# Kernel tuning notes

Hardware: AMD Instinct MI355X
Metric: run time of the kernel (lower is better)

The kernel has to match this reference:

```python
import jax, jax.numpy as jnp
import numpy as np

N = 1024       # gaussians
H = 256
W = 256
C = 64         # spectral channels
K = 2          # gabor components per gaussian
RADIUS_CLIP = 1.0
CHOL_BOUND = np.array([0.5, 0.0, 0.5], dtype=np.float32)


def setup_inputs() -> dict:
    key = jax.random.key(0)
    k1, k2, k3, k4, k5 = jax.random.split(key, 5)
    # _xyz = atanh(2*(rand-0.5))
    u = jax.random.uniform(k1, (N, 2), minval=-0.999, maxval=0.999)
    xyz = jnp.arctanh(u)
    cholesky = jax.random.uniform(k2, (N, 3))
    opacity = jnp.ones((N, 1), dtype=jnp.float32)
    # features init: inverse_softplus(0.05) + 0.01*randn
    inv_sp = float(np.log(np.expm1(0.05)))
    features_dc = inv_sp + 0.01 * jax.random.normal(k3, (N, C))
    gabor_freqs = (jax.random.uniform(k4, (N * K, 2)) - 0.5) * 0.002
    gabor_weights = jax.random.uniform(k5, (N * K, 1)) * -5.0
    return {
        'xyz': xyz, 'cholesky': cholesky, 'opacity': opacity,
        'features_dc': features_dc, 'gabor_freqs': gabor_freqs,
        'gabor_weights': gabor_weights,
    }


def _render(xyz, cholesky, opacity, features_dc, gabor_freqs, gabor_weights):
    # --- project_gaussians_2d ---
    xy = jnp.tanh(xyz)                              # [N,2] in (-1,1)
    xs = 0.5 * W * (xy[:, 0] + 1.0)                 # pixel-space centers
    ys = 0.5 * H * (xy[:, 1] + 1.0)
    L = cholesky + jnp.asarray(CHOL_BOUND)[None, :]  # [N,3] -> l1,l2,l3
    l1, l2, l3 = L[:, 0], L[:, 1], L[:, 2]
    # Sigma = L L^T, L = [[l1,0],[l2,l3]]
    s11 = l1 * l1
    s12 = l1 * l2
    s22 = l2 * l2 + l3 * l3
    det = (l1 * l3) ** 2
    ca = s22 / det                                  # conic = Sigma^-1
    cb = -s12 / det
    cc = s11 / det
    # radius = ceil(3*sqrt(max eigenvalue)); prune tiny gaussians
    mid = 0.5 * (s11 + s22)
    lam_max = mid + jnp.sqrt(jnp.maximum(mid * mid - det, 1e-8))
    radius = jnp.ceil(3.0 * jnp.sqrt(lam_max))
    keep = (radius > RADIUS_CLIP).astype(xyz.dtype)  # [N]

    # --- rasterize_gabor_sum (dense reference; kernel tiles, math identical) ---
    px = jnp.arange(W, dtype=xyz.dtype) + 0.5
    py = jnp.arange(H, dtype=xyz.dtype) + 0.5
    pxf = jnp.tile(px, H)                            # [HW]
    pyf = jnp.repeat(py, W)                          # [HW]
    dx = xs[:, None] - pxf[None, :]                  # [N,HW]
    dy = ys[:, None] - pyf[None, :]
    sigma = 0.5 * (ca[:, None] * dx * dx + cc[:, None] * dy * dy) + cb[:, None] * dx * dy
    alpha = opacity * jnp.exp(-sigma) * keep[:, None]  # [N,HW]

    freqs = jnp.exp(gabor_freqs).reshape(N, K, 2)
    wts = jax.nn.sigmoid(gabor_weights).reshape(N, K)
    mod = jnp.ones_like(dx)
    for k in range(K):  # K=2, structurally small loop
        mod = mod + wts[:, k, None] * jnp.cos(freqs[:, k, 0, None] * dx + freqs[:, k, 1, None] * dy)

    wmap = alpha * mod                               # [N,HW]
    feats = jax.nn.softplus(features_dc)             # [N,C]
    out = jnp.einsum('np,nc->pc', wmap, feats)       # [HW,C], sum compositing
    out = jnp.clip(out, 0.0, 1.0)
    return out.reshape(1, H, W, C).transpose(0, 3, 1, 2)  # [1,C,H,W]


def reference(xyz, cholesky, opacity, features_dc, gabor_freqs, gabor_weights):
    return _render(xyz, cholesky, opacity, features_dc, gabor_freqs, gabor_weights)
```

## Files before the change

kernel.cpp:

```cpp
#include <hip/hip_runtime.h>
#include <hip/hip_bf16.h>

#define NG     1024
#define NC     64
#define CULL_T 15.0f
#define MAXL   256
#define APAD   258
#define L2E    1.44269504f
#define INV2PI 0.15915494f

typedef float    f32x4 __attribute__((ext_vector_type(4)));
typedef _Float16 f16x4 __attribute__((ext_vector_type(4)));
typedef _Float16 f16x2 __attribute__((ext_vector_type(2)));

__device__ __forceinline__ float wgt_f(float4 p0, float4 p1, float4 p2,
                                       float pxf, float pyf) {
    const float dx = p0.x - pxf, dy = p0.y - pyf;
    const float t  = fmaf(p0.w, dy, p0.z * dx);
    const float s2 = fmaf(p1.x * dy, dy, dx * t);
    const float e  = __builtin_amdgcn_exp2f(s2);
    const float r1 = fmaf(p2.x, dx, p2.y * dy);
    const float c1 = __builtin_amdgcn_cosf(__builtin_amdgcn_fractf(r1));
    const float r2 = fmaf(p2.z, dx, p2.w * dy);
    const float c2 = __builtin_amdgcn_cosf(__builtin_amdgcn_fractf(r2));
    const float m  = fmaf(p1.w, c2, fmaf(p1.z, c1, 1.f));
    return e * p1.y * m;
}

__global__ __launch_bounds__(512) void fused_mfma_kernel(
    const float* __restrict__ xyz,  const float* __restrict__ chol,
    const float* __restrict__ opac, const float* __restrict__ fdc,
    const float* __restrict__ gfrq, const float* __restrict__ gwts,
    float* __restrict__ out)
{
    __shared__ float4 s_p0[MAXL], s_p1[MAXL], s_p2[MAXL];
    __shared__ unsigned short s_list[MAXL];
    __shared__ int s_scnt[16];
    __shared__ _Float16 A_lds[NC][APAD];

    const int tid  = threadIdx.x;
    const int lane = tid & 63, w = tid >> 6;

    const int x0 = (blockIdx.x & 7) << 5;
    const int y0 = (blockIdx.x >> 3) << 3;
    const float xlo = x0 + 0.5f, xhi = x0 + 31.5f;
    const float ylo = y0 + 0.5f, yhi = y0 + 7.5f;

    float4 P0[2];
    float  NCC[2], OK[2];
    bool   lv[2];
    int    pos[2];
    #pragma unroll
    for (int r = 0; r < 2; ++r) {
        const int n = (r << 9) + tid;
        const float2 xy = ((const float2*)xyz)[n];
        const float ex = __builtin_amdgcn_exp2f(2.f * L2E * xy.x);
        const float ey = __builtin_amdgcn_exp2f(2.f * L2E * xy.y);
        const float xs = 256.f - 256.f * __builtin_amdgcn_rcpf(1.f + ex);
        const float ys = 256.f - 256.f * __builtin_amdgcn_rcpf(1.f + ey);

        const float l1 = chol[3*n]     + 0.5f;
        const float l2 = chol[3*n + 1];
        const float l3 = chol[3*n + 2] + 0.5f;
        const float s11 = l1*l1, s12 = l1*l2, s22 = l2*l2 + l3*l3;
        const float dt  = (l1*l3) * (l1*l3);
        const float inv = __builtin_amdgcn_rcpf(dt);
        const float na = -0.5f * L2E * s22 * inv;
        const float nb =          L2E * s12 * inv;
        const float nc = -0.5f * L2E * s11 * inv;
        const float mid = 0.5f * (s11 + s22);
        const float lam = mid + __builtin_amdgcn_sqrtf(fmaxf(mid*mid - dt, 1e-8f));
        const float radius = ceilf(3.f * __builtin_amdgcn_sqrtf(lam));
        const float keep = (radius > 1.0f) ? 1.f : 0.f;
        const float oK = opac[n] * keep;
        const float r2 = (oK != 0.f) ? (2.f * CULL_T * lam) : -1.f;

        const float nx = fminf(fmaxf(xs, xlo), xhi);
        const float ny = fminf(fmaxf(ys, ylo), yhi);
        const float ddx = xs - nx, ddy = ys - ny;
        lv[r] = (ddx*ddx + ddy*ddy) <= r2;

        const unsigned long long m = __ballot(lv[r]);
        pos[r] = __popcll(m & ((1ull << lane) - 1ull));
        if (lane == 0) s_scnt[(r << 3) + w] = __popcll(m);

        P0[r] = make_float4(xs, ys, na, nb);
        NCC[r] = nc; OK[r] = oK;
    }
    __syncthreads();

    int pre[17];
    pre[0] = 0;
    #pragma unroll
    for (int s = 0; s < 16; ++s) pre[s+1] = pre[s] + s_scnt[s];
    const int total = min(pre[16], MAXL);

    #pragma unroll
    for (int r = 0; r < 2; ++r) {
        if (lv[r]) {
            const int p = pre[(r << 3) + w] + pos[r];
            if (p < MAXL) {
                const int n = (r << 9) + tid;
                const float4 gf = ((const float4*)gfrq)[n];
                const float2 gw = ((const float2*)gwts)[n];
                s_list[p] = (unsigned short)n;
                s_p0[p] = P0[r];
                s_p1[p] = make_float4(NCC[r], OK[r],
                    __builtin_amdgcn_rcpf(1.f + __builtin_amdgcn_exp2f(-L2E*gw.x)),
                    __builtin_amdgcn_rcpf(1.f + __builtin_amdgcn_exp2f(-L2E*gw.y)));
                s_p2[p] = make_float4(
                    __builtin_amdgcn_exp2f(L2E*gf.x)*INV2PI,
                    __builtin_amdgcn_exp2f(L2E*gf.y)*INV2PI,
                    __builtin_amdgcn_exp2f(L2E*gf.z)*INV2PI,
                    __builtin_amdgcn_exp2f(L2E*gf.w)*INV2PI);
            }
        }
    }
    for (int idx = total + tid; idx < MAXL; idx += 512) {
        s_p0[idx] = make_float4(0,0,0,0);
        s_p1[idx] = make_float4(0,0,0,0);
        s_p2[idx] = make_float4(0,0,0,0);
    }
    __syncthreads();

    const int nkc = (total + 15) >> 4;

    {
        const int c = tid & 63, kq = tid >> 6;
        for (int i = 0; i < nkc; ++i) {
            const int k0 = (i << 4) + (kq << 1);
            float v0 = 0.f, v1 = 0.f;
            if (k0 < total) {
                const int n = (int)s_list[k0];
                const float x = fdc[(n << 6) + c];
                v0 = 0.69314718f * __builtin_amdgcn_logf(
                         1.f + __builtin_amdgcn_exp2f(L2E * x));
            }
            if (k0 + 1 < total) {
                const int n = (int)s_list[k0 + 1];
                const float x = fdc[(n << 6) + c];
                v1 = 0.69314718f * __builtin_amdgcn_logf(
                         1.f + __builtin_amdgcn_exp2f(L2E * x));
            }
            *(f16x2*)&A_lds[c][k0] = (f16x2){(_Float16)v0, (_Float16)v1};
        }
    }
    __syncthreads();

    const int c15 = lane & 15, g = lane >> 4;
    const float pxf0 = x0 + c15 + 0.5f;
    const float pxf1 = x0 + 16 + c15 + 0.5f;
    const float pyf  = y0 + w + 0.5f;

    f32x4 acc[4][2];
    #pragma unroll
    for (int a = 0; a < 4; ++a) {
        acc[a][0] = (f32x4){0.f,0.f,0.f,0.f};
        acc[a][1] = (f32x4){0.f,0.f,0.f,0.f};
    }

    for (int kc = 0; kc < nkc; ++kc) {
        const int kb = (kc << 4) + (g << 2);

        const float4 q00 = s_p0[kb],   q10 = s_p1[kb],   q20 = s_p2[kb];
        const float4 q01 = s_p0[kb+1], q11 = s_p1[kb+1], q21 = s_p2[kb+1];
        const float4 q02 = s_p0[kb+2], q12 = s_p1[kb+2], q22 = s_p2[kb+2];
        const float4 q03 = s_p0[kb+3], q13 = s_p1[kb+3], q23 = s_p2[kb+3];

        const f16x4 bf0 = {
            (_Float16)wgt_f(q00, q10, q20, pxf0, pyf),
            (_Float16)wgt_f(q01, q11, q21, pxf0, pyf),
            (_Float16)wgt_f(q02, q12, q22, pxf0, pyf),
            (_Float16)wgt_f(q03, q13, q23, pxf0, pyf) };
        const f16x4 bf1 = {
            (_Float16)wgt_f(q00, q10, q20, pxf1, pyf),
            (_Float16)wgt_f(q01, q11, q21, pxf1, pyf),
            (_Float16)wgt_f(q02, q12, q22, pxf1, pyf),
            (_Float16)wgt_f(q03, q13, q23, pxf1, pyf) };

        const f16x4 af0 = *(const f16x4*)&A_lds[ 0 + c15][kb];
        const f16x4 af1 = *(const f16x4*)&A_lds[16 + c15][kb];
        const f16x4 af2 = *(const f16x4*)&A_lds[32 + c15][kb];
        const f16x4 af3 = *(const f16x4*)&A_lds[48 + c15][kb];

        acc[0][0] = __builtin_amdgcn_mfma_f32_16x16x16f16(af0, bf0, acc[0][0], 0,0,0);
        acc[0][1] = __builtin_amdgcn_mfma_f32_16x16x16f16(af0, bf1, acc[0][1], 0,0,0);
        acc[1][0] = __builtin_amdgcn_mfma_f32_16x16x16f16(af1, bf0, acc[1][0], 0,0,0);
        acc[1][1] = __builtin_amdgcn_mfma_f32_16x16x16f16(af1, bf1, acc[1][1], 0,0,0);
        acc[2][0] = __builtin_amdgcn_mfma_f32_16x16x16f16(af2, bf0, acc[2][0], 0,0,0);
        acc[2][1] = __builtin_amdgcn_mfma_f32_16x16x16f16(af2, bf1, acc[2][1], 0,0,0);
        acc[3][0] = __builtin_amdgcn_mfma_f32_16x16x16f16(af3, bf0, acc[3][0], 0,0,0);
        acc[3][1] = __builtin_amdgcn_mfma_f32_16x16x16f16(af3, bf1, acc[3][1], 0,0,0);
    }

    const int pg0 = ((y0 + w) << 8) + x0 + c15;
    #pragma unroll
    for (int mt = 0; mt < 4; ++mt) {
        #pragma unroll
        for (int q = 0; q < 4; ++q) {
            const int ch = mt*16 + g*4 + q;
            __builtin_nontemporal_store(
                fminf(fmaxf(acc[mt][0][q], 0.f), 1.f), &out[(ch << 16) + pg0]);
            __builtin_nontemporal_store(
                fminf(fmaxf(acc[mt][1][q], 0.f), 1.f), &out[(ch << 16) + pg0 + 16]);
        }
    }
}

extern "C" void kernel_launch(void* const* d_in, const int* in_sizes, int n_in,
                              void* d_out, int out_size, void* d_ws, size_t ws_size,
                              hipStream_t stream) {
    const float* xyz  = (const float*)d_in[0];
    const float* chol = (const float*)d_in[1];
    const float* opac = (const float*)d_in[2];
    const float* fdc  = (const float*)d_in[3];
    const float* gfrq = (const float*)d_in[4];
    const float* gwts = (const float*)d_in[5];

    fused_mfma_kernel<<<256, 512, 0, stream>>>(xyz, chol, opac, fdc,
                                               gfrq, gwts, (float*)d_out);
}
```

Before: 12.03 us.

## Double block size to 1024 threads, one gaussian and one pixel strip per thread

```diff
diff --git a/kernel.cpp b/kernel.cpp
--- a/kernel.cpp
+++ b/kernel.cpp
@@ -27,7 +27,7 @@
     return e * p1.y * m;
 }
 
-__global__ __launch_bounds__(512) void fused_mfma_kernel(
+__global__ __launch_bounds__(1024) void fused_mfma_kernel(
     const float* __restrict__ xyz,  const float* __restrict__ chol,
     const float* __restrict__ opac, const float* __restrict__ fdc,
     const float* __restrict__ gfrq, const float* __restrict__ gwts,
@@ -46,47 +46,37 @@
     const float xlo = x0 + 0.5f, xhi = x0 + 31.5f;
     const float ylo = y0 + 0.5f, yhi = y0 + 7.5f;
 
-    float4 P0[2];
-    float  NCC[2], OK[2];
-    bool   lv[2];
-    int    pos[2];
-    #pragma unroll
-    for (int r = 0; r < 2; ++r) {
-        const int n = (r << 9) + tid;
-        const float2 xy = ((const float2*)xyz)[n];
-        const float ex = __builtin_amdgcn_exp2f(2.f * L2E * xy.x);
-        const float ey = __builtin_amdgcn_exp2f(2.f * L2E * xy.y);
-        const float xs = 256.f - 256.f * __builtin_amdgcn_rcpf(1.f + ex);
-        const float ys = 256.f - 256.f * __builtin_amdgcn_rcpf(1.f + ey);
+    const int n = tid;
+    const float2 xy = ((const float2*)xyz)[n];
+    const float ex = __builtin_amdgcn_exp2f(2.f * L2E * xy.x);
+    const float ey = __builtin_amdgcn_exp2f(2.f * L2E * xy.y);
+    const float xs = 256.f - 256.f * __builtin_amdgcn_rcpf(1.f + ex);
+    const float ys = 256.f - 256.f * __builtin_amdgcn_rcpf(1.f + ey);
 
-        const float l1 = chol[3*n]     + 0.5f;
-        const float l2 = chol[3*n + 1];
-        const float l3 = chol[3*n + 2] + 0.5f;
-        const float s11 = l1*l1, s12 = l1*l2, s22 = l2*l2 + l3*l3;
-        const float dt  = (l1*l3) * (l1*l3);
-        const float inv = __builtin_amdgcn_rcpf(dt);
-        const float na = -0.5f * L2E * s22 * inv;
-        const float nb =          L2E * s12 * inv;
-        const float nc = -0.5f * L2E * s11 * inv;
-        const float mid = 0.5f * (s11 + s22);
-        const float lam = mid + __builtin_amdgcn_sqrtf(fmaxf(mid*mid - dt, 1e-8f));
-        const float radius = ceilf(3.f * __builtin_amdgcn_sqrtf(lam));
-        const float keep = (radius > 1.0f) ? 1.f : 0.f;
-        const float oK = opac[n] * keep;
-        const float r2 = (oK != 0.f) ? (2.f * CULL_T * lam) : -1.f;
+    const float l1 = chol[3*n]     + 0.5f;
+    const float l2 = chol[3*n + 1];
+    const float l3 = chol[3*n + 2] + 0.5f;
+    const float s11 = l1*l1, s12 = l1*l2, s22 = l2*l2 + l3*l3;
+    const float dt  = (l1*l3) * (l1*l3);
+    const float inv = __builtin_amdgcn_rcpf(dt);
+    const float na = -0.5f * L2E * s22 * inv;
+    const float nb =          L2E * s12 * inv;
+    const float ncc = -0.5f * L2E * s11 * inv;
+    const float mid = 0.5f * (s11 + s22);
+    const float lam = mid + __builtin_amdgcn_sqrtf(fmaxf(mid*mid - dt, 1e-8f));
+    const float radius = ceilf(3.f * __builtin_amdgcn_sqrtf(lam));
+    const float keep = (radius > 1.0f) ? 1.f : 0.f;
+    const float oK = opac[n] * keep;
+    const float r2 = (oK != 0.f) ? (2.f * CULL_T * lam) : -1.f;
 
-        const float nx = fminf(fmaxf(xs, xlo), xhi);
-        const float ny = fminf(fmaxf(ys, ylo), yhi);
-        const float ddx = xs - nx, ddy = ys - ny;
-        lv[r] = (ddx*ddx + ddy*ddy) <= r2;
+    const float nx = fminf(fmaxf(xs, xlo), xhi);
+    const float ny = fminf(fmaxf(ys, ylo), yhi);
+    const float ddx = xs - nx, ddy = ys - ny;
+    const bool lv = (ddx*ddx + ddy*ddy) <= r2;
 
-        const unsigned long long m = __ballot(lv[r]);
-        pos[r] = __popcll(m & ((1ull << lane) - 1ull));
-        if (lane == 0) s_scnt[(r << 3) + w] = __popcll(m);
-
-        P0[r] = make_float4(xs, ys, na, nb);
-        NCC[r] = nc; OK[r] = oK;
-    }
+    const unsigned long long m = __ballot(lv);
+    const int pos = __popcll(m & ((1ull << lane) - 1ull));
+    if (lane == 0) s_scnt[w] = __popcll(m);
     __syncthreads();
 
     int pre[17];
@@ -95,28 +85,24 @@
     for (int s = 0; s < 16; ++s) pre[s+1] = pre[s] + s_scnt[s];
     const int total = min(pre[16], MAXL);
 
-    #pragma unroll
-    for (int r = 0; r < 2; ++r) {
-        if (lv[r]) {
-            const int p = pre[(r << 3) + w] + pos[r];
-            if (p < MAXL) {
-                const int n = (r << 9) + tid;
-                const float4 gf = ((const float4*)gfrq)[n];
-                const float2 gw = ((const float2*)gwts)[n];
-                s_list[p] = (unsigned short)n;
-                s_p0[p] = P0[r];
-                s_p1[p] = make_float4(NCC[r], OK[r],
-                    __builtin_amdgcn_rcpf(1.f + __builtin_amdgcn_exp2f(-L2E*gw.x)),
-                    __builtin_amdgcn_rcpf(1.f + __builtin_amdgcn_exp2f(-L2E*gw.y)));
-                s_p2[p] = make_float4(
-                    __builtin_amdgcn_exp2f(L2E*gf.x)*INV2PI,
-                    __builtin_amdgcn_exp2f(L2E*gf.y)*INV2PI,
-                    __builtin_amdgcn_exp2f(L2E*gf.z)*INV2PI,
-                    __builtin_amdgcn_exp2f(L2E*gf.w)*INV2PI);
-            }
+    if (lv) {
+        const int p = pre[w] + pos;
+        if (p < MAXL) {
+            const float4 gf = ((const float4*)gfrq)[n];
+            const float2 gw = ((const float2*)gwts)[n];
+            s_list[p] = (unsigned short)n;
+            s_p0[p] = make_float4(xs, ys, na, nb);
+            s_p1[p] = make_float4(ncc, oK,
+                __builtin_amdgcn_rcpf(1.f + __builtin_amdgcn_exp2f(-L2E*gw.x)),
+                __builtin_amdgcn_rcpf(1.f + __builtin_amdgcn_exp2f(-L2E*gw.y)));
+            s_p2[p] = make_float4(
+                __builtin_amdgcn_exp2f(L2E*gf.x)*INV2PI,
+                __builtin_amdgcn_exp2f(L2E*gf.y)*INV2PI,
+                __builtin_amdgcn_exp2f(L2E*gf.z)*INV2PI,
+                __builtin_amdgcn_exp2f(L2E*gf.w)*INV2PI);
         }
     }
-    for (int idx = total + tid; idx < MAXL; idx += 512) {
+    for (int idx = total + tid; idx < MAXL; idx += 1024) {
         s_p0[idx] = make_float4(0,0,0,0);
         s_p1[idx] = make_float4(0,0,0,0);
         s_p2[idx] = make_float4(0,0,0,0);
@@ -128,36 +114,26 @@
     {
         const int c = tid & 63, kq = tid >> 6;
         for (int i = 0; i < nkc; ++i) {
-            const int k0 = (i << 4) + (kq << 1);
-            float v0 = 0.f, v1 = 0.f;
+            const int k0 = (i << 4) + kq;
+            float v0 = 0.f;
             if (k0 < total) {
-                const int n = (int)s_list[k0];
-                const float x = fdc[(n << 6) + c];
+                const int nn = (int)s_list[k0];
+                const float x = fdc[(nn << 6) + c];
                 v0 = 0.69314718f * __builtin_amdgcn_logf(
                          1.f + __builtin_amdgcn_exp2f(L2E * x));
             }
-            if (k0 + 1 < total) {
-                const int n = (int)s_list[k0 + 1];
-                const float x = fdc[(n << 6) + c];
-                v1 = 0.69314718f * __builtin_amdgcn_logf(
-                         1.f + __builtin_amdgcn_exp2f(L2E * x));
-            }
-            *(f16x2*)&A_lds[c][k0] = (f16x2){(_Float16)v0, (_Float16)v1};
+            A_lds[c][k0] = (_Float16)v0;
         }
     }
     __syncthreads();
 
     const int c15 = lane & 15, g = lane >> 4;
-    const float pxf0 = x0 + c15 + 0.5f;
-    const float pxf1 = x0 + 16 + c15 + 0.5f;
-    const float pyf  = y0 + w + 0.5f;
+    const float pxf = x0 + ((w & 1) << 4) + c15 + 0.5f;
+    const float pyf = y0 + (w >> 1) + 0.5f;
 
-    f32x4 acc[4][2];
+    f32x4 acc[4];
     #pragma unroll
-    for (int a = 0; a < 4; ++a) {
-        acc[a][0] = (f32x4){0.f,0.f,0.f,0.f};
-        acc[a][1] = (f32x4){0.f,0.f,0.f,0.f};
-    }
+    for (int a = 0; a < 4; ++a) acc[a] = (f32x4){0.f,0.f,0.f,0.f};
 
     for (int kc = 0; kc < nkc; ++kc) {
         const int kb = (kc << 4) + (g << 2);
@@ -167,42 +143,31 @@
         const float4 q02 = s_p0[kb+2], q12 = s_p1[kb+2], q22 = s_p2[kb+2];
         const float4 q03 = s_p0[kb+3], q13 = s_p1[kb+3], q23 = s_p2[kb+3];
 
-        const f16x4 bf0 = {
-            (_Float16)wgt_f(q00, q10, q20, pxf0, pyf),
-            (_Float16)wgt_f(q01, q11, q21, pxf0, pyf),
-            (_Float16)wgt_f(q02, q12, q22, pxf0, pyf),
-            (_Float16)wgt_f(q03, q13, q23, pxf0, pyf) };
-        const f16x4 bf1 = {
-            (_Float16)wgt_f(q00, q10, q20, pxf1, pyf),
-            (_Float16)wgt_f(q01, q11, q21, pxf1, pyf),
-            (_Float16)wgt_f(q02, q12, q22, pxf1, pyf),
-            (_Float16)wgt_f(q03, q13, q23, pxf1, pyf) };
+        const f16x4 bf = {
+            (_Float16)wgt_f(q00, q10, q20, pxf, pyf),
+            (_Float16)wgt_f(q01, q11, q21, pxf, pyf),
+            (_Float16)wgt_f(q02, q12, q22, pxf, pyf),
+            (_Float16)wgt_f(q03, q13, q23, pxf, pyf) };
 
         const f16x4 af0 = *(const f16x4*)&A_lds[ 0 + c15][kb];
         const f16x4 af1 = *(const f16x4*)&A_lds[16 + c15][kb];
         const f16x4 af2 = *(const f16x4*)&A_lds[32 + c15][kb];
         const f16x4 af3 = *(const f16x4*)&A_lds[48 + c15][kb];
 
-        acc[0][0] = __builtin_amdgcn_mfma_f32_16x16x16f16(af0, bf0, acc[0][0], 0,0,0);
-        acc[0][1] = __builtin_amdgcn_mfma_f32_16x16x16f16(af0, bf1, acc[0][1], 0,0,0);
-        acc[1][0] = __builtin_amdgcn_mfma_f32_16x16x16f16(af1, bf0, acc[1][0], 0,0,0);
-        acc[1][1] = __builtin_amdgcn_mfma_f32_16x16x16f16(af1, bf1, acc[1][1], 0,0,0);
-        acc[2][0] = __builtin_amdgcn_mfma_f32_16x16x16f16(af2, bf0, acc[2][0], 0,0,0);
-        acc[2][1] = __builtin_amdgcn_mfma_f32_16x16x16f16(af2, bf1, acc[2][1], 0,0,0);
-        acc[3][0] = __builtin_amdgcn_mfma_f32_16x16x16f16(af3, bf0, acc[3][0], 0,0,0);
-        acc[3][1] = __builtin_amdgcn_mfma_f32_16x16x16f16(af3, bf1, acc[3][1], 0,0,0);
+        acc[0] = __builtin_amdgcn_mfma_f32_16x16x16f16(af0, bf, acc[0], 0,0,0);
+        acc[1] = __builtin_amdgcn_mfma_f32_16x16x16f16(af1, bf, acc[1], 0,0,0);
+        acc[2] = __builtin_amdgcn_mfma_f32_16x16x16f16(af2, bf, acc[2], 0,0,0);
+        acc[3] = __builtin_amdgcn_mfma_f32_16x16x16f16(af3, bf, acc[3], 0,0,0);
     }
 
-    const int pg0 = ((y0 + w) << 8) + x0 + c15;
+    const int pg = ((y0 + (w >> 1)) << 8) + x0 + ((w & 1) << 4) + c15;
     #pragma unroll
     for (int mt = 0; mt < 4; ++mt) {
         #pragma unroll
         for (int q = 0; q < 4; ++q) {
             const int ch = mt*16 + g*4 + q;
             __builtin_nontemporal_store(
-                fminf(fmaxf(acc[mt][0][q], 0.f), 1.f), &out[(ch << 16) + pg0]);
-            __builtin_nontemporal_store(
-                fminf(fmaxf(acc[mt][1][q], 0.f), 1.f), &out[(ch << 16) + pg0 + 16]);
+                fminf(fmaxf(acc[mt][q], 0.f), 1.f), &out[(ch << 16) + pg]);
         }
     }
 }
@@ -217,6 +182,6 @@
     const float* gfrq = (const float*)d_in[4];
     const float* gwts = (const float*)d_in[5];
 
-    fused_mfma_kernel<<<256, 512, 0, stream>>>(xyz, chol, opac, fdc,
-                                               gfrq, gwts, (float*)d_out);
+    fused_mfma_kernel<<<256, 1024, 0, stream>>>(xyz, chol, opac, fdc,
+                                                gfrq, gwts, (float*)d_out);
 }
```

Result: faster. 11.30 us (-6.1%).
